# Kernel tuning notes

Hardware: AMD Instinct MI355X
Metric: run time of the kernel (lower is better)

## Reference

```python
import jax, jax.numpy as jnp
import numpy as np

N = 200000      # num nodes
TOPK = 32       # PPR neighbors kept per node
EMB = 64        # embedding dim


def setup_inputs() -> dict:
    key = jax.random.key(0)
    k1, k2, k3 = jax.random.split(key, 3)
    emb_table = jax.random.normal(k1, (N, EMB), dtype=jnp.float32)
    wei = jax.random.uniform(k2, (N, TOPK), dtype=jnp.float32)
    nei = jax.random.randint(k3, (N, TOPK), 0, N, dtype=jnp.int64)
    return {"emb_table": emb_table, "wei": wei, "nei": nei}


def reference(emb_table, wei, nei):
    # Weight preprocessing from __init__: binary mask of nonzero ppr weights,
    # row-normalized -> uniform weights over valid neighbors.
    w = jnp.where(wei == 0, 0.0, 1.0)                       # [N, topk]
    w = w / (jnp.sum(w, axis=-1, keepdims=True) + 1e-12)    # [N, topk]
    # forward: gather neighbor embeddings, weighted sum over topk.
    top_embs = emb_table[nei]                                # [N, topk, emb]
    out = jnp.einsum("nk,nke->ne", w, top_embs)             # [N, emb]
    return out[:, None, :]                                   # [N, 1, emb] like matmul(w[:,None,:], top_embs)
```

## Files before the change

### kernel.cpp

```cpp
#include <hip/hip_runtime.h>
#include <hip/hip_fp16.h>

#define TOPK 32
#define EMB 64

__global__ __launch_bounds__(256) void cvt_f32_to_f16(
    const float* __restrict__ src, __half* __restrict__ dst, int total4)
{
    int i = blockIdx.x * blockDim.x + threadIdx.x;
    if (i < total4) {
        float4 v = ((const float4*)src)[i];
        __half2 h0 = __floats2half2_rn(v.x, v.y);
        __half2 h1 = __floats2half2_rn(v.z, v.w);
        ((__half2*)dst)[i * 2]     = h0;
        ((__half2*)dst)[i * 2 + 1] = h1;
    }
}

__global__ __launch_bounds__(256) void pprgo_h_kernel(
    const __half* __restrict__ emb,
    const float*  __restrict__ wei,
    const int*    __restrict__ nei,
    float*        __restrict__ out,
    int n_nodes)
{
    const int tid  = blockIdx.x * blockDim.x + threadIdx.x;
    const int n    = tid >> 3;
    const int lane = tid & 7;
    if (n >= n_nodes) return;

    const long base = (long)n * TOPK;
    float w[4]; int idx[4];
    #pragma unroll
    for (int t = 0; t < 4; ++t) {
        w[t]   = wei[base + t * 8 + lane];
        idx[t] = nei[base + t * 8 + lane];
    }
    float m[4];
    #pragma unroll
    for (int t = 0; t < 4; ++t) m[t] = (w[t] != 0.0f) ? 1.0f : 0.0f;

    float acc[8] = {0.f, 0.f, 0.f, 0.f, 0.f, 0.f, 0.f, 0.f};
    float cnt = 0.0f;

    #pragma unroll
    for (int t = 0; t < 4; ++t) {
        int   j[8]; float a[8];
        #pragma unroll
        for (int k = 0; k < 8; ++k) {
            j[k] = __shfl(idx[t], k, 8);
            a[k] = __shfl(m[t],   k, 8);
        }
        float4 r[8];
        #pragma unroll
        for (int k = 0; k < 8; ++k) {
            r[k] = *(const float4*)(emb + (size_t)j[k] * EMB + lane * 8);
        }
        #pragma unroll
        for (int k = 0; k < 8; ++k) {
            const __half2* hp = (const __half2*)&r[k];
            #pragma unroll
            for (int q = 0; q < 4; ++q) {
                float2 f = __half22float2(hp[q]);
                acc[q * 2]     += a[k] * f.x;
                acc[q * 2 + 1] += a[k] * f.y;
            }
            cnt += a[k];
        }
    }

    const float s = 1.0f / (cnt + 1e-12f);
    float4 o0, o1;
    o0.x = acc[0] * s; o0.y = acc[1] * s; o0.z = acc[2] * s; o0.w = acc[3] * s;
    o1.x = acc[4] * s; o1.y = acc[5] * s; o1.z = acc[6] * s; o1.w = acc[7] * s;
    float* op = out + (size_t)n * EMB + lane * 8;
    *(float4*)op       = o0;
    *(float4*)(op + 4) = o1;
}

__global__ __launch_bounds__(256) void pprgo_f32_kernel(
    const float* __restrict__ emb,
    const float* __restrict__ wei,
    const int*   __restrict__ nei,
    float*       __restrict__ out,
    int n_nodes)
{
    const int tid   = blockIdx.x * blockDim.x + threadIdx.x;
    const int group = tid >> 4;
    const int lane  = tid & 15;
    if (group >= n_nodes) return;
    const int n = group;
    const long base = (long)n * TOPK;
    const float w0 = wei[base + lane];
    const float w1 = wei[base + 16 + lane];
    const int   i0 = nei[base + lane];
    const int   i1 = nei[base + 16 + lane];
    const float m0 = (w0 != 0.0f) ? 1.0f : 0.0f;
    const float m1 = (w1 != 0.0f) ? 1.0f : 0.0f;
    float4 acc = make_float4(0.f, 0.f, 0.f, 0.f);
    float  cnt = 0.0f;
    #pragma unroll 8
    for (int k = 0; k < 16; ++k) {
        const int   j0 = __shfl(i0, k, 16);
        const float a0 = __shfl(m0, k, 16);
        const float4 r0 = *(const float4*)(emb + (size_t)j0 * EMB + lane * 4);
        acc.x += a0 * r0.x; acc.y += a0 * r0.y; acc.z += a0 * r0.z; acc.w += a0 * r0.w;
        cnt += a0;
        const int   j1 = __shfl(i1, k, 16);
        const float a1 = __shfl(m1, k, 16);
        const float4 r1 = *(const float4*)(emb + (size_t)j1 * EMB + lane * 4);
        acc.x += a1 * r1.x; acc.y += a1 * r1.y; acc.z += a1 * r1.z; acc.w += a1 * r1.w;
        cnt += a1;
    }
    const float s = 1.0f / (cnt + 1e-12f);
    float4 o;
    o.x = acc.x * s; o.y = acc.y * s; o.z = acc.z * s; o.w = acc.w * s;
    *(float4*)(out + (size_t)n * EMB + lane * 4) = o;
}

extern "C" void kernel_launch(void* const* d_in, const int* in_sizes, int n_in,
                              void* d_out, int out_size, void* d_ws, size_t ws_size,
                              hipStream_t stream) {
    const float* emb = (const float*)d_in[0];
    const float* wei = (const float*)d_in[1];
    const int*   nei = (const int*)d_in[2];
    float*       out = (float*)d_out;

    const int n_nodes = in_sizes[1] / TOPK;
    const size_t need = (size_t)n_nodes * EMB * sizeof(__half);

    if (ws_size >= need) {
        __half* embh = (__half*)d_ws;
        const int total4 = n_nodes * EMB / 4;
        const int cvt_blocks = (total4 + 255) / 256;
        cvt_f32_to_f16<<<cvt_blocks, 256, 0, stream>>>(emb, embh, total4);

        const int threads = n_nodes * 8;
        const int blocks = (threads + 255) / 256;
        pprgo_h_kernel<<<blocks, 256, 0, stream>>>(embh, wei, nei, out, n_nodes);
    } else {
        const int threads = n_nodes * 16;
        const int blocks = (threads + 255) / 256;
        pprgo_f32_kernel<<<blocks, 256, 0, stream>>>(emb, wei, nei, out, n_nodes);
    }
}
```

Before: 233.7 us.

## Slice fp16 embedding table by feature chunk and transpose neighbor indices

Adds a prep kernel that converts the embedding table to fp16 and stores it as 8 feature-slice regions of 16 bytes per node. It also transposes neighbor indices, redirects masked neighbors to a zero sentinel row, and precomputes per-node normalization scales. The gather kernel then assigns each block to a single slice, so each slice's working set (about 3.2 MB) is small enough to sit in cache while the random gathers run, and each thread reads coalesced transposed indices with no shuffles or multiplies. In exchange it needs more workspace and extra writes of the transposed indices, and every index is reread once per slice.

```diff
diff --git a/kernel.cpp b/kernel.cpp
--- a/kernel.cpp
+++ b/kernel.cpp
@@ -3,6 +3,119 @@
 
 #define TOPK 32
 #define EMB 64
+#define NSLICE 8
+
+__global__ __launch_bounds__(256) void prep_kernel(
+    const float* __restrict__ emb,
+    const float* __restrict__ wei,
+    const int*   __restrict__ nei,
+    __half* __restrict__ embT,
+    int*    __restrict__ neiT,
+    float*  __restrict__ scale,
+    int n_nodes, int a_blocks, int b_blocks)
+{
+    const int t = threadIdx.x;
+    const size_t regionHalfs = (size_t)(n_nodes + 1) * 8;
+
+    if ((int)blockIdx.x < a_blocks) {
+        const int base = blockIdx.x * 64;
+        __shared__ __half lds[64 * 72];
+        const float4* src = (const float4*)emb + (size_t)base * 16;
+        #pragma unroll
+        for (int i = 0; i < 4; ++i) {
+            const int f = t + 256 * i;
+            const int nl = f >> 4, part = f & 15;
+            if (base + nl < n_nodes) {
+                float4 v = src[f];
+                __half2 h0 = __floats2half2_rn(v.x, v.y);
+                __half2 h1 = __floats2half2_rn(v.z, v.w);
+                *(__half2*)(&lds[nl * 72 + part * 4])     = h0;
+                *(__half2*)(&lds[nl * 72 + part * 4 + 2]) = h1;
+            }
+        }
+        __syncthreads();
+        #pragma unroll
+        for (int i = 0; i < 2; ++i) {
+            const int w = t + 256 * i;
+            const int s = w >> 6, nl = w & 63;
+            if (base + nl < n_nodes) {
+                float4 v = *(const float4*)(&lds[nl * 72 + s * 8]);
+                *(float4*)(embT + (size_t)s * regionHalfs + (size_t)(base + nl) * 8) = v;
+            }
+        }
+    } else if ((int)blockIdx.x < a_blocks + b_blocks) {
+        const int n = ((int)blockIdx.x - a_blocks) * 256 + t;
+        if (n < n_nodes) {
+            const int4*   nrow = (const int4*)(nei + (size_t)n * TOPK);
+            const float4* wrow = (const float4*)(wei + (size_t)n * TOPK);
+            float cnt = 0.0f;
+            #pragma unroll
+            for (int q = 0; q < 8; ++q) {
+                int4   j4 = nrow[q];
+                float4 w4 = wrow[q];
+                int o0 = (w4.x != 0.0f) ? j4.x : n_nodes; cnt += (w4.x != 0.0f) ? 1.0f : 0.0f;
+                int o1 = (w4.y != 0.0f) ? j4.y : n_nodes; cnt += (w4.y != 0.0f) ? 1.0f : 0.0f;
+                int o2 = (w4.z != 0.0f) ? j4.z : n_nodes; cnt += (w4.z != 0.0f) ? 1.0f : 0.0f;
+                int o3 = (w4.w != 0.0f) ? j4.w : n_nodes; cnt += (w4.w != 0.0f) ? 1.0f : 0.0f;
+                neiT[(size_t)(q * 4 + 0) * n_nodes + n] = o0;
+                neiT[(size_t)(q * 4 + 1) * n_nodes + n] = o1;
+                neiT[(size_t)(q * 4 + 2) * n_nodes + n] = o2;
+                neiT[(size_t)(q * 4 + 3) * n_nodes + n] = o3;
+            }
+            scale[n] = 1.0f / (cnt + 1e-12f);
+        }
+    } else {
+        if (t < NSLICE) {
+            float4 z = make_float4(0.f, 0.f, 0.f, 0.f);
+            *(float4*)(embT + (size_t)t * regionHalfs + (size_t)n_nodes * 8) = z;
+        }
+    }
+}
+
+__global__ __launch_bounds__(256) void gather_sliced_kernel(
+    const __half* __restrict__ embT,
+    const int*    __restrict__ neiT,
+    const float*  __restrict__ scale,
+    float*        __restrict__ out,
+    int n_nodes)
+{
+    const int s = blockIdx.x & 7;
+    const int n = ((int)blockIdx.x >> 3) * 256 + threadIdx.x;
+    if (n >= n_nodes) return;
+
+    const __half* region = embT + (size_t)s * (size_t)(n_nodes + 1) * 8;
+
+    float acc[8] = {0.f, 0.f, 0.f, 0.f, 0.f, 0.f, 0.f, 0.f};
+    #pragma unroll
+    for (int b = 0; b < 4; ++b) {
+        int idx[8];
+        #pragma unroll
+        for (int k = 0; k < 8; ++k)
+            idx[k] = neiT[(size_t)(b * 8 + k) * n_nodes + n];
+        float4 r[8];
+        #pragma unroll
+        for (int k = 0; k < 8; ++k)
+            r[k] = *(const float4*)(region + (size_t)idx[k] * 8);
+        #pragma unroll
+        for (int k = 0; k < 8; ++k) {
+            const __half2* hp = (const __half2*)&r[k];
+            #pragma unroll
+            for (int q = 0; q < 4; ++q) {
+                float2 f = __half22float2(hp[q]);
+                acc[q * 2]     += f.x;
+                acc[q * 2 + 1] += f.y;
+            }
+        }
+    }
+
+    const float sc = scale[n];
+    float4 o0, o1;
+    o0.x = acc[0] * sc; o0.y = acc[1] * sc; o0.z = acc[2] * sc; o0.w = acc[3] * sc;
+    o1.x = acc[4] * sc; o1.y = acc[5] * sc; o1.z = acc[6] * sc; o1.w = acc[7] * sc;
+    float* op = out + (size_t)n * EMB + s * 8;
+    *(float4*)op       = o0;
+    *(float4*)(op + 4) = o1;
+}
 
 __global__ __launch_bounds__(256) void cvt_f32_to_f16(
     const float* __restrict__ src, __half* __restrict__ dst, int total4)
@@ -10,10 +123,8 @@
     int i = blockIdx.x * blockDim.x + threadIdx.x;
     if (i < total4) {
         float4 v = ((const float4*)src)[i];
-        __half2 h0 = __floats2half2_rn(v.x, v.y);
-        __half2 h1 = __floats2half2_rn(v.z, v.w);
-        ((__half2*)dst)[i * 2]     = h0;
-        ((__half2*)dst)[i * 2 + 1] = h1;
+        ((__half2*)dst)[i * 2]     = __floats2half2_rn(v.x, v.y);
+        ((__half2*)dst)[i * 2 + 1] = __floats2half2_rn(v.z, v.w);
     }
 }
 
@@ -28,7 +139,6 @@
     const int n    = tid >> 3;
     const int lane = tid & 7;
     if (n >= n_nodes) return;
-
     const long base = (long)n * TOPK;
     float w[4]; int idx[4];
     #pragma unroll
@@ -39,43 +149,33 @@
     float m[4];
     #pragma unroll
     for (int t = 0; t < 4; ++t) m[t] = (w[t] != 0.0f) ? 1.0f : 0.0f;
-
-    float acc[8] = {0.f, 0.f, 0.f, 0.f, 0.f, 0.f, 0.f, 0.f};
+    float acc[8] = {0.f,0.f,0.f,0.f,0.f,0.f,0.f,0.f};
     float cnt = 0.0f;
-
     #pragma unroll
     for (int t = 0; t < 4; ++t) {
-        int   j[8]; float a[8];
-        #pragma unroll
-        for (int k = 0; k < 8; ++k) {
-            j[k] = __shfl(idx[t], k, 8);
-            a[k] = __shfl(m[t],   k, 8);
-        }
+        int j[8]; float a[8];
+        #pragma unroll
+        for (int k = 0; k < 8; ++k) { j[k] = __shfl(idx[t], k, 8); a[k] = __shfl(m[t], k, 8); }
         float4 r[8];
         #pragma unroll
-        for (int k = 0; k < 8; ++k) {
-            r[k] = *(const float4*)(emb + (size_t)j[k] * EMB + lane * 8);
-        }
+        for (int k = 0; k < 8; ++k) r[k] = *(const float4*)(emb + (size_t)j[k] * EMB + lane * 8);
         #pragma unroll
         for (int k = 0; k < 8; ++k) {
             const __half2* hp = (const __half2*)&r[k];
             #pragma unroll
             for (int q = 0; q < 4; ++q) {
                 float2 f = __half22float2(hp[q]);
-                acc[q * 2]     += a[k] * f.x;
-                acc[q * 2 + 1] += a[k] * f.y;
+                acc[q*2] += a[k]*f.x; acc[q*2+1] += a[k]*f.y;
             }
             cnt += a[k];
         }
     }
-
-    const float s = 1.0f / (cnt + 1e-12f);
+    const float sc = 1.0f / (cnt + 1e-12f);
     float4 o0, o1;
-    o0.x = acc[0] * s; o0.y = acc[1] * s; o0.z = acc[2] * s; o0.w = acc[3] * s;
-    o1.x = acc[4] * s; o1.y = acc[5] * s; o1.z = acc[6] * s; o1.w = acc[7] * s;
+    o0.x=acc[0]*sc; o0.y=acc[1]*sc; o0.z=acc[2]*sc; o0.w=acc[3]*sc;
+    o1.x=acc[4]*sc; o1.y=acc[5]*sc; o1.z=acc[6]*sc; o1.w=acc[7]*sc;
     float* op = out + (size_t)n * EMB + lane * 8;
-    *(float4*)op       = o0;
-    *(float4*)(op + 4) = o1;
+    *(float4*)op = o0; *(float4*)(op+4) = o1;
 }
 
 __global__ __launch_bounds__(256) void pprgo_f32_kernel(
@@ -89,33 +189,30 @@
     const int group = tid >> 4;
     const int lane  = tid & 15;
     if (group >= n_nodes) return;
-    const int n = group;
-    const long base = (long)n * TOPK;
+    const long base = (long)group * TOPK;
     const float w0 = wei[base + lane];
     const float w1 = wei[base + 16 + lane];
     const int   i0 = nei[base + lane];
     const int   i1 = nei[base + 16 + lane];
     const float m0 = (w0 != 0.0f) ? 1.0f : 0.0f;
     const float m1 = (w1 != 0.0f) ? 1.0f : 0.0f;
-    float4 acc = make_float4(0.f, 0.f, 0.f, 0.f);
+    float4 acc = make_float4(0.f,0.f,0.f,0.f);
     float  cnt = 0.0f;
     #pragma unroll 8
     for (int k = 0; k < 16; ++k) {
         const int   j0 = __shfl(i0, k, 16);
         const float a0 = __shfl(m0, k, 16);
         const float4 r0 = *(const float4*)(emb + (size_t)j0 * EMB + lane * 4);
-        acc.x += a0 * r0.x; acc.y += a0 * r0.y; acc.z += a0 * r0.z; acc.w += a0 * r0.w;
-        cnt += a0;
+        acc.x += a0*r0.x; acc.y += a0*r0.y; acc.z += a0*r0.z; acc.w += a0*r0.w; cnt += a0;
         const int   j1 = __shfl(i1, k, 16);
         const float a1 = __shfl(m1, k, 16);
         const float4 r1 = *(const float4*)(emb + (size_t)j1 * EMB + lane * 4);
-        acc.x += a1 * r1.x; acc.y += a1 * r1.y; acc.z += a1 * r1.z; acc.w += a1 * r1.w;
-        cnt += a1;
-    }
-    const float s = 1.0f / (cnt + 1e-12f);
+        acc.x += a1*r1.x; acc.y += a1*r1.y; acc.z += a1*r1.z; acc.w += a1*r1.w; cnt += a1;
+    }
+    const float sc = 1.0f / (cnt + 1e-12f);
     float4 o;
-    o.x = acc.x * s; o.y = acc.y * s; o.z = acc.z * s; o.w = acc.w * s;
-    *(float4*)(out + (size_t)n * EMB + lane * 4) = o;
+    o.x=acc.x*sc; o.y=acc.y*sc; o.z=acc.z*sc; o.w=acc.w*sc;
+    *(float4*)(out + (size_t)group * EMB + lane * 4) = o;
 }
 
 extern "C" void kernel_launch(void* const* d_in, const int* in_sizes, int n_in,
@@ -127,20 +224,35 @@
     float*       out = (float*)d_out;
 
     const int n_nodes = in_sizes[1] / TOPK;
-    const size_t need = (size_t)n_nodes * EMB * sizeof(__half);
-
-    if (ws_size >= need) {
+
+    const size_t embT_bytes  = (size_t)NSLICE * (size_t)(n_nodes + 1) * 8 * sizeof(__half);
+    const size_t neiT_bytes  = (size_t)TOPK * n_nodes * sizeof(int);
+    const size_t scale_bytes = (size_t)n_nodes * sizeof(float);
+    const size_t need_sliced = embT_bytes + neiT_bytes + scale_bytes;
+    const size_t need_h      = (size_t)n_nodes * EMB * sizeof(__half);
+
+    if (ws_size >= need_sliced) {
+        __half* embT  = (__half*)d_ws;
+        int*    neiT  = (int*)((char*)d_ws + embT_bytes);
+        float*  scale = (float*)((char*)d_ws + embT_bytes + neiT_bytes);
+
+        const int a_blocks = (n_nodes + 63) / 64;
+        const int b_blocks = (n_nodes + 255) / 256;
+        const int prep_blocks = a_blocks + b_blocks + 1;
+        prep_kernel<<<prep_blocks, 256, 0, stream>>>(
+            emb, wei, nei, embT, neiT, scale, n_nodes, a_blocks, b_blocks);
+
+        const int gather_blocks = NSLICE * ((n_nodes + 255) / 256);
+        gather_sliced_kernel<<<gather_blocks, 256, 0, stream>>>(
+            embT, neiT, scale, out, n_nodes);
+    } else if (ws_size >= need_h) {
         __half* embh = (__half*)d_ws;
         const int total4 = n_nodes * EMB / 4;
-        const int cvt_blocks = (total4 + 255) / 256;
-        cvt_f32_to_f16<<<cvt_blocks, 256, 0, stream>>>(emb, embh, total4);
-
+        cvt_f32_to_f16<<<(total4 + 255) / 256, 256, 0, stream>>>(emb, embh, total4);
         const int threads = n_nodes * 8;
-        const int blocks = (threads + 255) / 256;
-        pprgo_h_kernel<<<blocks, 256, 0, stream>>>(embh, wei, nei, out, n_nodes);
+        pprgo_h_kernel<<<(threads + 255) / 256, 256, 0, stream>>>(embh, wei, nei, out, n_nodes);
     } else {
         const int threads = n_nodes * 16;
-        const int blocks = (threads + 255) / 256;
-        pprgo_f32_kernel<<<blocks, 256, 0, stream>>>(emb, wei, nei, out, n_nodes);
-    }
-}
+        pprgo_f32_kernel<<<(threads + 255) / 256, 256, 0, stream>>>(emb, wei, nei, out, n_nodes);
+    }
+}
```

Measured after the change: 395.6 us. +69.3%, slower.
